# Performance work log

Hardware: AMD Instinct MI355X
Metric: run time of the kernel (lower is better)

## Reference

```python
import jax, jax.numpy as jnp
import numpy as np

B, DEPTH, H, I = 8, 12, 512, 512
N = 2**DEPTH - 1  # 4095 nodes, complete binary tree (heap indexed)


def setup_inputs() -> dict:
    key = jax.random.key(0)
    ks = jax.random.split(key, 9)
    s_i = 1.0 / np.sqrt(I)
    s_h = 1.0 / np.sqrt(H)
    u = lambda k, shape, s: jax.random.uniform(k, shape, jnp.float32, -s, s)
    return {
        "inputs": jax.random.normal(ks[0], (B, N, I), jnp.float32),
        "depth": DEPTH,
        # torch Linear weights stored as [in, out] (already transposed)
        "W_gih": u(ks[1], (I, 3 * H), s_i),
        "b_gih": u(ks[2], (3 * H,), s_i),
        "W_glhh": u(ks[3], (H, 3 * H), s_h),
        "W_grhh": u(ks[4], (H, 3 * H), s_h),
        "W_cih": u(ks[5], (I, H), s_i),
        "b_cih": u(ks[6], (H,), s_i),
        "W_clhh": u(ks[7], (H, H), s_h),
        "W_crhh": u(ks[8], (H, H), s_h),
    }


def reference(inputs, depth, W_gih, b_gih, W_glhh, W_grhh, W_cih, b_cih, W_clhh, W_crhh):
    b, n, _ = inputs.shape
    h_dim = W_clhh.shape[0]
    # Input-dependent affines for every node, computed once (big GEMMs up front).
    gx = inputs @ W_gih + b_gih            # [B, N, 3H]
    cx = inputs @ W_cih + b_cih            # [B, N, H]

    def node_forward(gx_n, cx_n, lh, rh):
        # gates = sigmoid(gate_ih(x) + gate_lhh(lh) + gate_rhh(rh))
        gates = jax.nn.sigmoid(gx_n + lh @ W_glhh + rh @ W_grhh)
        rp, zp, z = jnp.split(gates, 3, axis=-1)
        cell = jnp.tanh(cx_n + (rp * lh) @ W_clhh + (rp * rh) @ W_crhh)
        return zp * (lh + rh) + z * cell

    h = jnp.zeros((b, n, h_dim), inputs.dtype)
    # root (node 0): both parent states are zeros
    z0 = jnp.zeros((b, h_dim), inputs.dtype)
    h = h.at[:, 0].set(node_forward(gx[:, 0], cx[:, 0], z0, z0))
    # top-down over levels; heap tree: parent(i)=(i-1)//2, odd index => left child
    for d in range(1, depth):
        start, end = 2 ** d - 1, 2 ** (d + 1) - 1
        idx = jnp.arange(start, end)
        parent = (idx - 1) // 2
        ph = h[:, parent]                          # [B, L, H] gather parent states
        is_left = (idx % 2 == 1)[None, :, None]
        lh = jnp.where(is_left, ph, jnp.zeros_like(ph))
        rh = jnp.where(is_left, jnp.zeros_like(ph), ph)
        h = h.at[:, start:end].set(node_forward(gx[:, start:end], cx[:, start:end], lh, rh))

    # original output ordering: nodes 1..N-1 then root; output_t = root state
    outputs = jnp.concatenate([h[:, 1:], h[:, :1]], axis=1)  # [B, N, H]
    return outputs, h[:, 0]
```

## Files before the change

kernel.cpp:

```cpp
#include <hip/hip_runtime.h>
#include <hip/hip_bf16.h>
#include <cstdint>
#include <cstddef>

#define BATCH   8
#define NNODES  4095
#define HD      512
#define ID      512
#define LDG     1536
#define MAXR    8192

typedef unsigned short ushort_t;
typedef __attribute__((ext_vector_type(8))) short  bf16x8;
typedef __attribute__((ext_vector_type(4))) float  f32x4;

__device__ __forceinline__ float bf2f(unsigned short u){
  union { uint32_t i; float f; } v; v.i = ((uint32_t)u) << 16; return v.f;
}
__device__ __forceinline__ unsigned short f2bf(float f){
  union { float f; uint32_t i; } v; v.f = f;
  uint32_t r = v.i + 0x7fffu + ((v.i >> 16) & 1u);
  return (unsigned short)(r >> 16);
}
__device__ __forceinline__ float sigm(float x){ return 1.0f/(1.0f + __expf(-x)); }
__device__ __forceinline__ float tanh_(float x){ return 1.0f - 2.0f/(__expf(2.0f*x)+1.0f); }

#define GLOAD16(g, l) __builtin_amdgcn_global_load_lds(                      \
    (const __attribute__((address_space(1))) void*)(g),                      \
    (__attribute__((address_space(3))) void*)(l), 16, 0, 0)

#define WAIT_VM(N)  asm volatile("s_waitcnt vmcnt(" #N ")" ::: "memory")
#define WAIT_LGKM0  asm volatile("s_waitcnt lgkmcnt(0)" ::: "memory")
#define SBAR        __builtin_amdgcn_s_barrier()
#define SCHEDB      __builtin_amdgcn_sched_barrier(0)

__device__ __forceinline__ int xcd_swz(int orig, int nwg){
  return (orig & 7) * (nwg >> 3) + (orig >> 3);
}



__global__ __launch_bounds__(256)
void prep_gather(const float* __restrict__ X, ushort_t* __restrict__ Abf,
                 const float* __restrict__ Wg_ih, const float* __restrict__ Wc_ih,
                 const float* __restrict__ Wg_l,  const float* __restrict__ Wg_r,
                 const float* __restrict__ Wc_l,  const float* __restrict__ Wc_r,
                 ushort_t* __restrict__ WgTih, ushort_t* __restrict__ WcTih,
                 ushort_t* __restrict__ WgThh, ushort_t* __restrict__ WcThh)
{
  __shared__ float t[64][65];
  const int bid = blockIdx.x;
  if (bid < 16380){
    const size_t i = (size_t)bid*256 + threadIdx.x;
    const int row = (int)(i >> 7);
    const int c4  = ((int)i & 127)*4;
    const int node = row >> 3, b = row & 7;
    float4 v = *(const float4*)&X[((size_t)b*NNODES + node)*ID + c4];
    ushort4 o = { f2bf(v.x), f2bf(v.y), f2bf(v.z), f2bf(v.w) };
    *(ushort4*)&Abf[(size_t)row*512 + c4] = o;
    return;
  }
  const int pid  = bid - 16380;
  const int px   = pid % 24;
  const int py   = (pid / 24) & 7;
  const int zsel = pid / 192;
  const float* W; ushort_t* D; int N;
  switch (zsel){
    case 0: W = Wg_ih; D = WgTih;                        N = 1536; break;
    case 1: W = Wc_ih; D = WcTih;                        N = 512;  break;
    case 2: W = Wg_l;  D = WgThh;                        N = 1536; break;
    case 3: W = Wg_r;  D = WgThh + (size_t)1536*512;     N = 1536; break;
    case 4: W = Wc_l;  D = WcThh;                        N = 512;  break;
    default:W = Wc_r;  D = WcThh + (size_t)512*512;      N = 512;  break;
  }
  const int n0 = px*64;
  if (n0 >= N) return;
  const int k0 = py*64;
  const int c = threadIdx.x & 63, rq = threadIdx.x >> 6;
  #pragma unroll
  for (int q = 0; q < 16; ++q){
    int r = q*4 + rq;
    t[r][c] = W[(size_t)(k0 + r)*N + n0 + c];
  }
  __syncthreads();
  #pragma unroll
  for (int q = 0; q < 16; ++q){
    int r = q*4 + rq;
    D[(size_t)(n0 + r)*512 + k0 + c] = f2bf(t[c][r]);
  }
}


#define READ_A(BUF, IH)                                                        \
  _Pragma("unroll") for (int i2_ = 0; i2_ < 4; ++i2_){                         \
    const int row_ = wr*128 + (IH)*64 + i2_*16 + fr;                           \
    _Pragma("unroll") for (int s_ = 0; s_ < 2; ++s_)                           \
      af[i2_][s_] = *(const bf16x8*)&Al[BUF][s_][row_][sl*8];                  \
  }

#define READ_B(BUF, JH, DST)                                                   \
  _Pragma("unroll") for (int j2_ = 0; j2_ < 2; ++j2_){                         \
    const int row_ = wc*64 + (JH)*32 + j2_*16 + fr;                            \
    _Pragma("unroll") for (int s_ = 0; s_ < 2; ++s_)                           \
      DST[j2_][s_] = *(const bf16x8*)&Bl[BUF][s_][row_][sl*8];                 \
  }

#define EXEC(IH, JH, BFR, STAGE_STMT, WAIT_STMT) do {                          \
  STAGE_STMT;                                                                  \
  SBAR;                                                                        \
  WAIT_LGKM0; SCHEDB;                                                          \
  __builtin_amdgcn_s_setprio(1);                                               \
  _Pragma("unroll") for (int i2_ = 0; i2_ < 4; ++i2_)                          \
    _Pragma("unroll") for (int j2_ = 0; j2_ < 2; ++j2_)                        \
      _Pragma("unroll") for (int s_ = 0; s_ < 2; ++s_)                         \
        acc[(IH)*4+i2_][(JH)*2+j2_] = __builtin_amdgcn_mfma_f32_16x16x32_bf16( \
            af[i2_][s_], BFR[j2_][s_], acc[(IH)*4+i2_][(JH)*2+j2_], 0,0,0);    \
  __builtin_amdgcn_s_setprio(0);                                               \
  WAIT_STMT;                                                                   \
  SCHEDB; SBAR;                                                                \
} while(0)

__global__ __launch_bounds__(512, 2)
void gemm_hoist(const ushort_t* __restrict__ A,
                const ushort_t* __restrict__ BTg, const float* __restrict__ bg,
                ushort_t* __restrict__ Gx,
                const ushort_t* __restrict__ BTc, const float* __restrict__ bc,
                ushort_t* __restrict__ Cx)
{
  __shared__ __align__(16) ushort_t SH[65536];
  ushort_t (*Al)[2][256][32] = (ushort_t (*)[2][256][32])SH;
  ushort_t (*Bl)[2][256][32] = (ushort_t (*)[2][256][32])(SH + 32768);
  const int wg = xcd_swz(blockIdx.x, gridDim.x);
  const ushort_t* BT; const float* bias; ushort_t* C; int N, m0, n0;
  if (wg < 768){ BT = BTg; bias = bg; C = Gx; N = 1536;
                 m0 = (wg/6)*256; n0 = (wg%6)*256; }
  else         { BT = BTc; bias = bc; C = Cx; N = 512;
                 const int t = wg - 768; m0 = (t>>1)*256; n0 = (t&1)*256; }
  const int tid = threadIdx.x, lane = tid & 63, wave = tid >> 6;
  const ushort_t* Abase = A + (size_t)m0*512;
  const ushort_t* Bbase = BT + (size_t)n0*512;
  const int wr = wave >> 2, wc = wave & 3;
  const int fr = lane & 15, fq = lane >> 4;
  const int lr = lane >> 2;
  const int cs = ((lane & 3) - (lr >> 1)) & 3;
  const size_t lo = (size_t)lr*512 + (size_t)cs*8;
  const int sl = (fq + (fr >> 1)) & 3;
  f32x4 acc[8][4] = {};
  bf16x8 af[4][2], bf0[2][2], bf1[2][2];

  auto stageA = [&](int buf, int h, int T){
    const int k0 = T*64;
    #pragma unroll
    for (int q = 0; q < 2; ++q){
      const int idx = wave*2 + q;
      const int s   = idx & 1;
      const int rb  = idx >> 1;
      const int r0  = (rb >> 2)*128 + h*64 + (rb & 3)*16;
      GLOAD16(Abase + (size_t)r0*512 + k0 + s*32 + lo, &Al[buf][s][r0][0]);
    }
  };
  auto stageB = [&](int buf, int h, int T){
    const int k0 = T*64;
    #pragma unroll
    for (int q = 0; q < 2; ++q){
      const int idx = wave*2 + q;
      const int s   = idx & 1;
      const int rb  = idx >> 1;
      const int r0  = (rb >> 1)*64 + h*32 + (rb & 1)*16;
      GLOAD16(Bbase + (size_t)r0*512 + k0 + s*32 + lo, &Bl[buf][s][r0][0]);
    }
  };

  stageA(0,0,0); stageB(0,0,0); stageA(0,1,0); stageB(0,1,0);
  stageA(1,0,1); stageB(1,0,1);
  WAIT_VM(4); SCHEDB; SBAR;

  for (int it = 0; it < 4; ++it){
    const int T1 = 2*it + 1, T2 = 2*it + 2, T3 = 2*it + 3;
    const bool more = (it < 3);
    READ_A(0,0); READ_B(0,0,bf0);
    EXEC(0,0,bf0, stageA(1,1,T1), (void)0);
    READ_B(0,1,bf1);
    EXEC(0,1,bf1, stageB(1,1,T1), (void)0);
    READ_A(0,1);
    EXEC(1,1,bf1, if(more) stageA(0,0,T2), (void)0);
    EXEC(1,0,bf0, if(more) stageB(0,0,T2),
                  if(more){ WAIT_VM(4); } else { WAIT_VM(0); });
    READ_A(1,0); READ_B(1,0,bf0);
    EXEC(0,0,bf0, if(more) stageA(0,1,T2), (void)0);
    READ_B(1,1,bf1);
    EXEC(0,1,bf1, if(more) stageB(0,1,T2), (void)0);
    READ_A(1,1);
    EXEC(1,1,bf1, if(more) stageA(1,0,T3), (void)0);
    EXEC(1,0,bf0, if(more) stageB(1,0,T3),
                  if(more){ WAIT_VM(4); } else { WAIT_VM(0); });
  }

  float* CT = (float*)SH;
  const int er = tid >> 3;
  const int ec = tid & 7;
  #pragma unroll
  for (int p = 0; p < 4; ++p){
    __syncthreads();
    #pragma unroll
    for (int i2 = 0; i2 < 2; ++i2){
      const int i = p*2 + i2;
      #pragma unroll
      for (int j = 0; j < 4; ++j){
        const int cc = wc*64 + j*16 + fr;
        const float bv = bias[n0 + cc];
        #pragma unroll
        for (int r = 0; r < 4; ++r){
          const int crow = wr*32 + i2*16 + fq*4 + r;
          CT[crow*256 + (cc ^ ((crow & 7) << 2))] = acc[i][j][r] + bv;
        }
      }
    }
    __syncthreads();
    const int grow = m0 + p*32 + (er >> 5)*128 + (er & 31);
    ushort_t* Crow = C + (size_t)grow*N + n0;
    const int rx = (er & 7) << 2;
    #pragma unroll
    for (int q = 0; q < 8; ++q){
      const int c0 = ec*4 + q*32;
      float4 v = *(const float4*)&CT[er*256 + (c0 ^ rx)];
      ushort4 o = { f2bf(v.x), f2bf(v.y), f2bf(v.z), f2bf(v.w) };
      *(ushort4*)&Crow[c0] = o;
    }
  }
}

__global__ __launch_bounds__(256)
void gates_rp(const ushort_t* __restrict__ Hprev, const ushort_t* __restrict__ WgThh,
              const ushort_t* __restrict__ Gx, ushort_t* __restrict__ Ubuf, int s)
{
  __shared__ __align__(16) ushort_t Al[3][128][32];
  __shared__ __align__(16) ushort_t Bl[3][128][32];
  const int wg = xcd_swz(blockIdx.x, gridDim.x);
  const int n0 = (wg & 3)*128;
  const int z  = (wg >> 2) & 1;
  const int m0 = (wg >> 3)*128;
  const int tid = threadIdx.x, lane = tid & 63, wave = tid >> 6;
  const ushort_t* Abase = Hprev + (size_t)m0*512;
  const ushort_t* Bbase = WgThh + ((size_t)z*1536 + n0)*512;
  const int wr = wave >> 1, wc = wave & 1;
  const int fr = lane & 15, fq = lane >> 4;
  const int lr = lane >> 2;
  const int cs = ((lane & 3) - (lr >> 1)) & 3;
  const size_t lo = (size_t)lr*512 + cs*8;
  const int sl = (fq + (fr >> 1)) & 3;
  f32x4 acc[4][4] = {};

  auto stage = [&](int buf, int kt){
    const int k0 = kt*32;
    #pragma unroll
    for (int q = 0; q < 2; ++q){
      int r = q*64 + wave*16;
      GLOAD16(Abase + (size_t)r*512 + k0 + lo, &Al[buf][r][0]);
      GLOAD16(Bbase + (size_t)r*512 + k0 + lo, &Bl[buf][r][0]);
    }
  };

  stage(0, 0); stage(1, 1); stage(2, 2);
  WAIT_VM(4); SCHEDB; SBAR;
  for (int it = 0; it < 8; ++it){
    const int cur = (2*it) % 3, nxt = (2*it + 1) % 3;
    bf16x8 af[4], bfr[4];
    #pragma unroll
    for (int i = 0; i < 4; i++){
      af[i]  = *(const bf16x8*)&Al[cur][wr*64 + i*16 + fr][sl*8];
      bfr[i] = *(const bf16x8*)&Bl[cur][wc*64 + i*16 + fr][sl*8];
    }
    WAIT_LGKM0; SCHEDB;
    __builtin_amdgcn_s_setprio(1);
    #pragma unroll
    for (int i = 0; i < 4; i++)
      #pragma unroll
      for (int j = 0; j < 4; j++)
        acc[i][j] = __builtin_amdgcn_mfma_f32_16x16x32_bf16(af[i], bfr[j], acc[i][j], 0,0,0);
    __builtin_amdgcn_s_setprio(0);
    #pragma unroll
    for (int i = 0; i < 4; i++){
      af[i]  = *(const bf16x8*)&Al[nxt][wr*64 + i*16 + fr][sl*8];
      bfr[i] = *(const bf16x8*)&Bl[nxt][wc*64 + i*16 + fr][sl*8];
    }
    WAIT_LGKM0; SCHEDB; SBAR;
    if (2*it + 3 < 16) stage(cur, 2*it + 3);
    if (2*it + 4 < 16) stage(nxt, 2*it + 4);
    __builtin_amdgcn_s_setprio(1);
    #pragma unroll
    for (int i = 0; i < 4; i++)
      #pragma unroll
      for (int j = 0; j < 4; j++)
        acc[i][j] = __builtin_amdgcn_mfma_f32_16x16x32_bf16(af[i], bfr[j], acc[i][j], 0,0,0);
    __builtin_amdgcn_s_setprio(0);
    if (2*it + 4 < 16){ WAIT_VM(4); } else { WAIT_VM(0); }
    SCHEDB; SBAR;
  }

  #pragma unroll
  for (int i = 0; i < 4; i++)
    #pragma unroll
    for (int j = 0; j < 4; j++){
      const int col = n0 + wc*64 + j*16 + fr;
      #pragma unroll
      for (int r = 0; r < 4; r++){
        const int m = m0 + wr*64 + i*16 + fq*4 + r;
        const int t = m >> 3, b = m & 7;
        const int node = s + 2*t + z;
        const float gx = bf2f(Gx[(size_t)(node*8 + b)*1536 + col]);
        const float ph = bf2f(Hprev[(size_t)m*512 + col]);
        Ubuf[((size_t)z*MAXR + m)*512 + col] = f2bf(sigm(acc[i][j][r] + gx) * ph);
      }
    }
}

__global__ __launch_bounds__(256)
void cell_comb(const ushort_t* __restrict__ Ubuf, const ushort_t* __restrict__ Hprev,
               const ushort_t* __restrict__ WcThh, const ushort_t* __restrict__ WgThh,
               const ushort_t* __restrict__ Gx, const ushort_t* __restrict__ Cx,
               float* __restrict__ out, ushort_t* __restrict__ Hcur,
               int s, int writeH)
{
  __shared__ __align__(16) ushort_t Ul[2][128][32];
  __shared__ __align__(16) ushort_t Hl[2][128][32];
  __shared__ __align__(16) ushort_t Bc[2][64][32];
  __shared__ __align__(16) ushort_t Bp[2][64][32];
  __shared__ __align__(16) ushort_t Bz[2][64][32];
  const int wg = xcd_swz(blockIdx.x, gridDim.x);
  const int n0 = (wg & 7)*64;
  const int z  = (wg >> 3) & 1;
  const int m0 = (wg >> 4)*128;
  const int tid = threadIdx.x, lane = tid & 63, wave = tid >> 6;
  const int wr = wave >> 1, wc = wave & 1;
  const int fr = lane & 15, fq = lane >> 4;
  const int lr = lane >> 2;
  const int cs = ((lane & 3) - (lr >> 1)) & 3;
  const int lc = cs*8;
  const int sl = (fq + (fr >> 1)) & 3;

  const ushort_t* Ab  = Ubuf  + ((size_t)z*MAXR + m0)*512;
  const ushort_t* Hb  = Hprev + (size_t)m0*512;
  const ushort_t* Bcb = WcThh + ((size_t)z*512  + n0)*512;
  const ushort_t* Bpb = WgThh + ((size_t)z*1536 + 512  + n0)*512;
  const ushort_t* Bzb = WgThh + ((size_t)z*1536 + 1024 + n0)*512;

  f32x4 acc_c[4][2] = {}, acc_p[4][2] = {}, acc_z[4][2] = {};

  auto stage = [&](int buf, int kt){
    const int k0 = kt*32;
    #pragma unroll
    for (int q = 0; q < 2; ++q){
      const int r = q*64 + wave*16;
      GLOAD16(Ab + (size_t)(r + lr)*512 + k0 + lc, &Ul[buf][r][0]);
      GLOAD16(Hb + (size_t)(r + lr)*512 + k0 + lc, &Hl[buf][r][0]);
    }
    const int r2 = wave*16;
    GLOAD16(Bcb + (size_t)(r2 + lr)*512 + k0 + lc, &Bc[buf][r2][0]);
    GLOAD16(Bpb + (size_t)(r2 + lr)*512 + k0 + lc, &Bp[buf][r2][0]);
    GLOAD16(Bzb + (size_t)(r2 + lr)*512 + k0 + lc, &Bz[buf][r2][0]);
  };

  stage(0, 0); stage(1, 1);
  WAIT_VM(7); SCHEDB; SBAR;
  int cur = 0;
  for (int kt = 0; kt < 16; ++kt){
    bf16x8 au[4], ah[4], bc2[2], bp2[2], bz2[2];
    #pragma unroll
    for (int i = 0; i < 4; i++){
      au[i] = *(const bf16x8*)&Ul[cur][wr*64 + i*16 + fr][sl*8];
      ah[i] = *(const bf16x8*)&Hl[cur][wr*64 + i*16 + fr][sl*8];
    }
    #pragma unroll
    for (int j = 0; j < 2; j++){
      bc2[j] = *(const bf16x8*)&Bc[cur][wc*32 + j*16 + fr][sl*8];
      bp2[j] = *(const bf16x8*)&Bp[cur][wc*32 + j*16 + fr][sl*8];
      bz2[j] = *(const bf16x8*)&Bz[cur][wc*32 + j*16 + fr][sl*8];
    }
    __builtin_amdgcn_s_setprio(1);
    #pragma unroll
    for (int i = 0; i < 4; i++)
      #pragma unroll
      for (int j = 0; j < 2; j++){
        acc_c[i][j] = __builtin_amdgcn_mfma_f32_16x16x32_bf16(au[i], bc2[j], acc_c[i][j], 0,0,0);
        acc_p[i][j] = __builtin_amdgcn_mfma_f32_16x16x32_bf16(ah[i], bp2[j], acc_p[i][j], 0,0,0);
        acc_z[i][j] = __builtin_amdgcn_mfma_f32_16x16x32_bf16(ah[i], bz2[j], acc_z[i][j], 0,0,0);
      }
    __builtin_amdgcn_s_setprio(0);
    WAIT_LGKM0; SCHEDB; SBAR; SCHEDB;
    if (kt < 14) stage(cur, kt+2);
    if (kt < 14) { WAIT_VM(7); } else { WAIT_VM(0); }
    SCHEDB; SBAR;
    cur ^= 1;
  }

  #pragma unroll
  for (int i = 0; i < 4; i++)
    #pragma unroll
    for (int j = 0; j < 2; j++){
      const int col = n0 + wc*32 + j*16 + fr;
      #pragma unroll
      for (int r = 0; r < 4; r++){
        const int m = m0 + wr*64 + i*16 + fq*4 + r;
        const int t = m >> 3, b = m & 7;
        const int node = s + 2*t + z;
        const size_t crow = (size_t)node*8 + b;
        const float cell = tanh_(acc_c[i][j][r] + bf2f(Cx[crow*512 + col]));
        const float zp   = sigm(acc_p[i][j][r] + bf2f(Gx[crow*1536 + 512  + col]));
        const float zv   = sigm(acc_z[i][j][r] + bf2f(Gx[crow*1536 + 1024 + col]));
        const float ph = bf2f(Hprev[(size_t)m*512 + col]);
        const float h  = zp*ph + zv*cell;
        out[((size_t)b*NNODES + node - 1)*HD + col] = h;
        if (writeH) Hcur[(size_t)((2*t + z)*8 + b)*512 + col] = f2bf(h);
      }
    }
}

__global__ void root_k(const ushort_t* __restrict__ Gx, const ushort_t* __restrict__ Cx,
                       float* __restrict__ out, ushort_t* __restrict__ H0)
{
  const int b = blockIdx.x, c = threadIdx.x;
  float zv   = sigm(bf2f(Gx[(size_t)b*1536 + 1024 + c]));
  float cell = tanh_(bf2f(Cx[(size_t)b*512 + c]));
  float h = zv * cell;
  out[((size_t)b*NNODES + (NNODES-1))*HD + c] = h;
  out[(size_t)BATCH*NNODES*HD + (size_t)b*HD + c] = h;
  H0[(size_t)b*512 + c] = f2bf(h);
}

__global__ __launch_bounds__(1024)
void small_gates2(const ushort_t* __restrict__ Hprev, const ushort_t* __restrict__ Gx,
    const float* __restrict__ Wg_l, const float* __restrict__ Wg_r,
    float* __restrict__ G, float* __restrict__ Uf, int s)
{
  __shared__ float PHl[8][512];
  __shared__ float red[8][8][128];
  const int t = blockIdx.x, node = s + t;
  const int tid  = threadIdx.x;
  const int colq = tid & 127;
  const int ks   = tid >> 7;
  const int col  = blockIdx.y*128 + colq;
  const int prow0 = (t >> 1)*8;
  for (int idx = tid; idx < 8*512; idx += 1024){
    int b = idx >> 9, k = idx & 511;
    PHl[b][k] = bf2f(Hprev[(size_t)(prow0 + b)*512 + k]);
  }
  __syncthreads();
  const float* Whh = (node & 1) ? Wg_l : Wg_r;
  float acc[8] = {};
  const int k0 = ks << 6;
  #pragma unroll 8
  for (int k = 0; k < 64; k++){
    float w = Whh[(size_t)(k0 + k)*LDG + col];
    #pragma unroll
    for (int b = 0; b < 8; b++) acc[b] = fmaf(PHl[b][k0 + k], w, acc[b]);
  }
  #pragma unroll
  for (int b = 0; b < 8; b++) red[ks][b][colq] = acc[b];
  __syncthreads();
  if (ks == 0){
    #pragma unroll
    for (int b = 0; b < 8; b++){
      float a = bf2f(Gx[(size_t)(node*8 + b)*1536 + col]);
      #pragma unroll
      for (int q = 0; q < 8; q++) a += red[q][b][colq];
      float g = sigm(a);
      G[((size_t)(t*8 + b))*1536 + col] = g;
      if (col < 512) Uf[((size_t)(t*8 + b))*512 + col] = g * PHl[b][col];
    }
  }
}

__global__ __launch_bounds__(1024)
void small_cell2(float* __restrict__ out, const ushort_t* __restrict__ Cx,
    const float* __restrict__ Wc_l, const float* __restrict__ Wc_r,
    const float* __restrict__ G, const float* __restrict__ Uf,
    const ushort_t* __restrict__ Hprev, ushort_t* __restrict__ Hcur, int s)
{
  __shared__ float Ul[8][512];
  __shared__ float red[8][8][128];
  const int t = blockIdx.x, node = s + t;
  const int tid  = threadIdx.x;
  const int colq = tid & 127;
  const int ks   = tid >> 7;
  const int col  = blockIdx.y*128 + colq;
  for (int idx = tid; idx < 8*512; idx += 1024){
    int b = idx >> 9, k = idx & 511;
    Ul[b][k] = Uf[((size_t)(t*8 + b))*512 + k];
  }
  __syncthreads();
  const float* Whh = (node & 1) ? Wc_l : Wc_r;
  float acc[8] = {};
  const int k0 = ks << 6;
  #pragma unroll 8
  for (int k = 0; k < 64; k++){
    float w = Whh[(size_t)(k0 + k)*HD + col];
    #pragma unroll
    for (int b = 0; b < 8; b++) acc[b] = fmaf(Ul[b][k0 + k], w, acc[b]);
  }
  #pragma unroll
  for (int b = 0; b < 8; b++) red[ks][b][colq] = acc[b];
  __syncthreads();
  if (ks == 0){
    const int prow0 = (t >> 1)*8;
    #pragma unroll
    for (int b = 0; b < 8; b++){
      float a = bf2f(Cx[(size_t)(node*8 + b)*512 + col]);
      #pragma unroll
      for (int q = 0; q < 8; q++) a += red[q][b][colq];
      float zp = G[((size_t)(t*8 + b))*1536 + 512  + col];
      float zv = G[((size_t)(t*8 + b))*1536 + 1024 + col];
      float ph = bf2f(Hprev[(size_t)(prow0 + b)*512 + col]);
      float h  = zp*ph + zv*tanh_(a);
      out[((size_t)b*NNODES + (node - 1))*HD + col] = h;
      Hcur[(size_t)(t*8 + b)*512 + col] = f2bf(h);
    }
  }
}

__device__ __forceinline__ void unpack8(uint4 u, float v[8]){
  v[0]=bf2f((unsigned short)(u.x & 0xffffu)); v[1]=bf2f((unsigned short)(u.x >> 16));
  v[2]=bf2f((unsigned short)(u.y & 0xffffu)); v[3]=bf2f((unsigned short)(u.y >> 16));
  v[4]=bf2f((unsigned short)(u.z & 0xffffu)); v[5]=bf2f((unsigned short)(u.z >> 16));
  v[6]=bf2f((unsigned short)(u.w & 0xffffu)); v[7]=bf2f((unsigned short)(u.w >> 16));
}
__device__ __forceinline__ void gemm_acc(const unsigned short* Al0,
                                         const unsigned short* Al1,
                                         const float* __restrict__ W,
                                         int ldw, int c0, float acc[2][16])
{
  const float* wr = W + c0;
  #pragma unroll 2
  for (int k0 = 0; k0 < 512; k0 += 8){
    uint4 u0 = *(const uint4*)(Al0 + k0);
    uint4 u1 = *(const uint4*)(Al1 + k0);
    float a0[8], a1[8];
    unpack8(u0, a0); unpack8(u1, a1);
    #pragma unroll
    for (int kk = 0; kk < 8; kk++){
      float wv[16];
      *(float4*)(wv+ 0) = *(const float4*)(wr+ 0);
      *(float4*)(wv+ 4) = *(const float4*)(wr+ 4);
      *(float4*)(wv+ 8) = *(const float4*)(wr+ 8);
      *(float4*)(wv+12) = *(const float4*)(wr+12);
      wr += ldw;
      float x0 = a0[kk], x1 = a1[kk];
      #pragma unroll
      for (int j = 0; j < 16; j++){
        acc[0][j] = fmaf(x0, wv[j], acc[0][j]);
        acc[1][j] = fmaf(x1, wv[j], acc[1][j]);
      }
    }
  }
}

__global__ __launch_bounds__(256)
void tdtree_level(const float* __restrict__ X, float* __restrict__ out,
    const float* __restrict__ Wg_ih, const float* __restrict__ bg,
    const float* __restrict__ Wg_l,  const float* __restrict__ Wg_r,
    const float* __restrict__ Wc_ih, const float* __restrict__ bc,
    const float* __restrict__ Wc_l,  const float* __restrict__ Wc_r,
    int s, int nodes_p, int isRoot)
{
  __shared__ __align__(16) unsigned short Xl [16][512];
  __shared__ __align__(16) unsigned short PHl[16][512];
  __shared__ __align__(16) unsigned short Ul [16][512];

  const int tid = threadIdx.x;
  const int tx  = tid & 31;
  const int ty  = tid >> 5;
  const int parity = blockIdx.y;
  const float* Wg_hh = parity ? Wg_r : Wg_l;
  const float* Wc_hh = parity ? Wc_r : Wc_l;
  const int t0 = blockIdx.x * 2;

  for (int idx = tid; idx < 16*512; idx += 256){
    int m = idx >> 9, k = idx & 511;
    int t = t0 + (m >> 3), b = m & 7;
    float xv = 0.f, pv = 0.f;
    if (t < nodes_p){
      int node = isRoot ? 0 : (s + 2*t + parity);
      xv = X[((size_t)b*NNODES + node)*ID + k];
      if (!isRoot){
        int pnode = (node - 1) >> 1;
        int pslot = pnode ? (pnode - 1) : (NNODES - 1);
        pv = out[((size_t)b*NNODES + pslot)*HD + k];
      }
    }
    Xl[m][k]  = f2bf(xv);
    PHl[m][k] = f2bf(pv);
  }
  __syncthreads();

  const int r0 = ty*2, r1 = r0 + 1;
  const int c  = tx*16;
  const unsigned short* Ax0 = &Xl[r0][0];
  const unsigned short* Ax1 = &Xl[r1][0];
  const unsigned short* Ap0 = &PHl[r0][0];
  const unsigned short* Ap1 = &PHl[r1][0];
  float acc[2][16], cell[2][16];

  #pragma unroll
  for (int j=0;j<16;j++){ float bv = bg[c+j]; acc[0][j]=bv; acc[1][j]=bv; }
  gemm_acc(Ax0, Ax1, Wg_ih, LDG, c, acc);
  if (!isRoot) gemm_acc(Ap0, Ap1, Wg_hh, LDG, c, acc);
  #pragma unroll
  for (int j=0;j<16;j++){
    Ul[r0][c+j] = f2bf(sigm(acc[0][j]) * bf2f(PHl[r0][c+j]));
    Ul[r1][c+j] = f2bf(sigm(acc[1][j]) * bf2f(PHl[r1][c+j]));
  }
  __syncthreads();

  #pragma unroll
  for (int j=0;j<16;j++){ float bv = bc[c+j]; cell[0][j]=bv; cell[1][j]=bv; }
  gemm_acc(Ax0, Ax1, Wc_ih, HD, c, cell);
  if (!isRoot) gemm_acc(&Ul[r0][0], &Ul[r1][0], Wc_hh, HD, c, cell);
  #pragma unroll
  for (int j=0;j<16;j++){ cell[0][j] = tanh_(cell[0][j]); cell[1][j] = tanh_(cell[1][j]); }

  #pragma unroll
  for (int j=0;j<16;j++){ float bv = bg[1024+c+j]; acc[0][j]=bv; acc[1][j]=bv; }
  gemm_acc(Ax0, Ax1, Wg_ih, LDG, 1024+c, acc);
  if (!isRoot) gemm_acc(Ap0, Ap1, Wg_hh, LDG, 1024+c, acc);
  #pragma unroll
  for (int j=0;j<16;j++){ cell[0][j] *= sigm(acc[0][j]); cell[1][j] *= sigm(acc[1][j]); }

  #pragma unroll
  for (int j=0;j<16;j++){ float bv = bg[512+c+j]; acc[0][j]=bv; acc[1][j]=bv; }
  gemm_acc(Ax0, Ax1, Wg_ih, LDG, 512+c, acc);
  if (!isRoot) gemm_acc(Ap0, Ap1, Wg_hh, LDG, 512+c, acc);

  #pragma unroll
  for (int i=0;i<2;i++){
    int m = r0 + i;
    int t = t0 + (m >> 3), b = m & 7;
    if (t >= nodes_p) continue;
    int node = isRoot ? 0 : (s + 2*t + parity);
    int slot = node ? (node - 1) : (NNODES - 1);
    float* op = out + ((size_t)b*NNODES + slot)*HD + c;
    float hv[16];
    if (isRoot){
      #pragma unroll
      for (int j=0;j<16;j++) hv[j] = cell[i][j];
    } else {
      int pnode = (node - 1) >> 1;
      int pslot = pnode ? (pnode - 1) : (NNODES - 1);
      const float* pp = out + ((size_t)b*NNODES + pslot)*HD + c;
      #pragma unroll
      for (int j=0;j<16;j++) hv[j] = sigm(acc[i][j]) * pp[j] + cell[i][j];
    }
    #pragma unroll
    for (int q=0;q<4;q++) *(float4*)(op + q*4) = *(const float4*)(hv + q*4);
    if (isRoot){
      float* o2 = out + (size_t)BATCH*NNODES*HD + (size_t)b*HD + c;
      #pragma unroll
      for (int q=0;q<4;q++) *(float4*)(o2 + q*4) = *(const float4*)(hv + q*4);
    }
  }
}

extern "C" void kernel_launch(void* const* d_in, const int* in_sizes, int n_in,
                              void* d_out, int out_size, void* d_ws, size_t ws_size,
                              hipStream_t stream)
{
  const float* X     = (const float*)d_in[0];
  const float* Wg_ih = (const float*)d_in[2];
  const float* bg    = (const float*)d_in[3];
  const float* Wg_l  = (const float*)d_in[4];
  const float* Wg_r  = (const float*)d_in[5];
  const float* Wc_ih = (const float*)d_in[6];
  const float* bc    = (const float*)d_in[7];
  const float* Wc_l  = (const float*)d_in[8];
  const float* Wc_r  = (const float*)d_in[9];
  float* out = (float*)d_out;
  char* ws = (char*)d_ws;

  size_t o = 0;
  ushort_t* WgTih = (ushort_t*)(ws + o); o += (size_t)1536*512*2;
  ushort_t* WcTih = (ushort_t*)(ws + o); o += (size_t)512*512*2;
  ushort_t* WgThh = (ushort_t*)(ws + o); o += (size_t)3072*512*2;
  ushort_t* WcThh = (ushort_t*)(ws + o); o += (size_t)1024*512*2;
  ushort_t* Gxp   = (ushort_t*)(ws + o); o += (size_t)32768*1536*2;
  ushort_t* Cxp   = (ushort_t*)(ws + o); o += (size_t)32768*512*2;
  ushort_t* Hb0   = (ushort_t*)(ws + o); o += (size_t)MAXR*512*2;
  ushort_t* Hb1   = (ushort_t*)(ws + o); o += (size_t)MAXR*512*2;
  char*     BIG   = ws + o;              o += (size_t)32768*512*2;
  float*    Gs    = (float*)(ws + o);    o += (size_t)512*1536*4;
  float*    Us    = (float*)(ws + o);    o += (size_t)512*512*4;
  const size_t NEED = o;

  if (ws_size >= NEED){
    ushort_t* Abf  = (ushort_t*)BIG;
    ushort_t* Ubuf = (ushort_t*)BIG;

    prep_gather<<<dim3(16380 + 1152), 256, 0, stream>>>(
        X, Abf, Wg_ih, Wc_ih, Wg_l, Wg_r, Wc_l, Wc_r,
        WgTih, WcTih, WgThh, WcThh);
    gemm_hoist<<<dim3(1024), 512, 0, stream>>>(Abf, WgTih, bg, Gxp, WcTih, bc, Cxp);

    root_k<<<dim3(8), 512, 0, stream>>>(Gxp, Cxp, out, Hb0);

    for (int d = 1; d < 12; ++d){
      const int count = 1 << d, s = count - 1;
      ushort_t* Hprev = ((d-1) & 1) ? Hb1 : Hb0;
      ushort_t* Hcur  = (d & 1) ? Hb1 : Hb0;
      if (d < 7){
        small_gates2<<<dim3(count,12), 1024, 0, stream>>>(Hprev, Gxp, Wg_l, Wg_r, Gs, Us, s);
        small_cell2 <<<dim3(count,4),  1024, 0, stream>>>(out, Cxp, Wc_l, Wc_r, Gs, Us, Hprev, Hcur, s);
      } else {
        const int mt = 1 << (d - 5);
        gates_rp <<<dim3(mt*8),  256, 0, stream>>>(Hprev, WgThh, Gxp, Ubuf, s);
        cell_comb<<<dim3(mt*16), 256, 0, stream>>>(Ubuf, Hprev, WcThh, WgThh,
                                                   Gxp, Cxp, out, Hcur, s, d < 11);
      }
    }
    return;
  }

  for (int d = 0; d < 12; ++d){
    const int count  = 1 << d;
    const int snode  = count - 1;
    const int isRoot = (d == 0);
    const int nodes_p = isRoot ? 1 : (count >> 1);
    const int blocks  = (nodes_p + 1) >> 1;
    dim3 grid(blocks, isRoot ? 1 : 2);
    tdtree_level<<<grid, 256, 0, stream>>>(X, out, Wg_ih, bg, Wg_l, Wg_r,
                                           Wc_ih, bc, Wc_l, Wc_r,
                                           snode, nodes_p, isRoot);
  }
}
```

Baseline: 559.3 us.

## Triple-buffer activation tiles and unroll cell_comb K-loop by two

Restructures the cell_comb main loop. Activation tiles (U and H) move to a three-slot LDS ring while the weight tiles keep two slots, and the loop is unrolled so each iteration handles two K-steps. The second half's fragment reads and the next global loads are issued before the second MFMA batch, with one barrier per two K-steps. The aim is fewer barriers and more load/compute overlap; the cost is more LDS per block, which may lower occupancy, and more intricate wait-count bookkeeping.

```diff
diff --git a/kernel.cpp b/kernel.cpp
--- a/kernel.cpp
+++ b/kernel.cpp
@@ -322,8 +322,8 @@
                float* __restrict__ out, ushort_t* __restrict__ Hcur,
                int s, int writeH)
 {
-  __shared__ __align__(16) ushort_t Ul[2][128][32];
-  __shared__ __align__(16) ushort_t Hl[2][128][32];
+  __shared__ __align__(16) ushort_t Ul[3][128][32];
+  __shared__ __align__(16) ushort_t Hl[3][128][32];
   __shared__ __align__(16) ushort_t Bc[2][64][32];
   __shared__ __align__(16) ushort_t Bp[2][64][32];
   __shared__ __align__(16) ushort_t Bz[2][64][32];
@@ -347,7 +347,7 @@
 
   f32x4 acc_c[4][2] = {}, acc_p[4][2] = {}, acc_z[4][2] = {};
 
-  auto stage = [&](int buf, int kt){
+  auto stageA = [&](int buf, int kt){
     const int k0 = kt*32;
     #pragma unroll
     for (int q = 0; q < 2; ++q){
@@ -355,28 +355,39 @@
       GLOAD16(Ab + (size_t)(r + lr)*512 + k0 + lc, &Ul[buf][r][0]);
       GLOAD16(Hb + (size_t)(r + lr)*512 + k0 + lc, &Hl[buf][r][0]);
     }
+  };
+  auto stageB = [&](int buf, int kt){
+    const int k0 = kt*32;
     const int r2 = wave*16;
     GLOAD16(Bcb + (size_t)(r2 + lr)*512 + k0 + lc, &Bc[buf][r2][0]);
     GLOAD16(Bpb + (size_t)(r2 + lr)*512 + k0 + lc, &Bp[buf][r2][0]);
     GLOAD16(Bzb + (size_t)(r2 + lr)*512 + k0 + lc, &Bz[buf][r2][0]);
   };
 
-  stage(0, 0); stage(1, 1);
-  WAIT_VM(7); SCHEDB; SBAR;
-  int cur = 0;
-  for (int kt = 0; kt < 16; ++kt){
+  auto read_frags = [&](int abuf, int bbuf, bf16x8 au[4], bf16x8 ah[4],
+                        bf16x8 bc2[2], bf16x8 bp2[2], bf16x8 bz2[2]){
+    #pragma unroll
+    for (int i = 0; i < 4; i++){
+      au[i] = *(const bf16x8*)&Ul[abuf][wr*64 + i*16 + fr][sl*8];
+      ah[i] = *(const bf16x8*)&Hl[abuf][wr*64 + i*16 + fr][sl*8];
+    }
+    #pragma unroll
+    for (int j = 0; j < 2; j++){
+      bc2[j] = *(const bf16x8*)&Bc[bbuf][wc*32 + j*16 + fr][sl*8];
+      bp2[j] = *(const bf16x8*)&Bp[bbuf][wc*32 + j*16 + fr][sl*8];
+      bz2[j] = *(const bf16x8*)&Bz[bbuf][wc*32 + j*16 + fr][sl*8];
+    }
+  };
+
+  stageB(0, 0); stageB(1, 1);
+  stageA(0, 0); stageA(1, 1); stageA(2, 2);
+  WAIT_VM(4); SCHEDB; SBAR;
+
+  for (int it = 0; it < 8; ++it){
+    const int a0 = (2*it) % 3, a1 = (2*it + 1) % 3;
     bf16x8 au[4], ah[4], bc2[2], bp2[2], bz2[2];
-    #pragma unroll
-    for (int i = 0; i < 4; i++){
-      au[i] = *(const bf16x8*)&Ul[cur][wr*64 + i*16 + fr][sl*8];
-      ah[i] = *(const bf16x8*)&Hl[cur][wr*64 + i*16 + fr][sl*8];
-    }
-    #pragma unroll
-    for (int j = 0; j < 2; j++){
-      bc2[j] = *(const bf16x8*)&Bc[cur][wc*32 + j*16 + fr][sl*8];
-      bp2[j] = *(const bf16x8*)&Bp[cur][wc*32 + j*16 + fr][sl*8];
-      bz2[j] = *(const bf16x8*)&Bz[cur][wc*32 + j*16 + fr][sl*8];
-    }
+    read_frags(a0, 0, au, ah, bc2, bp2, bz2);
+    WAIT_LGKM0; SCHEDB;
     __builtin_amdgcn_s_setprio(1);
     #pragma unroll
     for (int i = 0; i < 4; i++)
@@ -387,11 +398,24 @@
         acc_z[i][j] = __builtin_amdgcn_mfma_f32_16x16x32_bf16(ah[i], bz2[j], acc_z[i][j], 0,0,0);
       }
     __builtin_amdgcn_s_setprio(0);
-    WAIT_LGKM0; SCHEDB; SBAR; SCHEDB;
-    if (kt < 14) stage(cur, kt+2);
-    if (kt < 14) { WAIT_VM(7); } else { WAIT_VM(0); }
+    read_frags(a1, 1, au, ah, bc2, bp2, bz2);
+    WAIT_LGKM0; SCHEDB; SBAR;
+    if (2*it + 2 < 16) stageB(0, 2*it + 2);
+    if (2*it + 3 < 16) stageB(1, 2*it + 3);
+    if (2*it + 3 < 16) stageA(a0, 2*it + 3);
+    if (2*it + 4 < 16) stageA(a1, 2*it + 4);
+    __builtin_amdgcn_s_setprio(1);
+    #pragma unroll
+    for (int i = 0; i < 4; i++)
+      #pragma unroll
+      for (int j = 0; j < 2; j++){
+        acc_c[i][j] = __builtin_amdgcn_mfma_f32_16x16x32_bf16(au[i], bc2[j], acc_c[i][j], 0,0,0);
+        acc_p[i][j] = __builtin_amdgcn_mfma_f32_16x16x32_bf16(ah[i], bp2[j], acc_p[i][j], 0,0,0);
+        acc_z[i][j] = __builtin_amdgcn_mfma_f32_16x16x32_bf16(ah[i], bz2[j], acc_z[i][j], 0,0,0);
+      }
+    __builtin_amdgcn_s_setprio(0);
+    if (2*it + 4 < 16){ WAIT_VM(4); } else { WAIT_VM(0); }
     SCHEDB; SBAR;
-    cur ^= 1;
   }
 
   #pragma unroll
```

Result: faster. 543.0 us (-2.9%).
